# Kernel optimization log

Hardware: AMD Instinct MI355X
Metric: run time of the kernel (lower is better)

The kernel has to match this reference:

```python
import jax, jax.numpy as jnp
import numpy as np

N_NODES = 100000
N_EDGES = 1600000
N_GRAPHS = 256
D = 128
L = 3
N_OUT = 10


def setup_inputs() -> dict:
    key = jax.random.key(0)
    ks = jax.random.split(key, 6)
    x = jax.random.normal(ks[0], (N_NODES, D), dtype=jnp.float32)
    edge_index = jax.random.randint(ks[1], (2, N_EDGES), 0, N_NODES, dtype=jnp.int64)
    batch = jnp.sort(jax.random.randint(ks[2], (N_NODES,), 0, N_GRAPHS, dtype=jnp.int64))
    conv_w = jax.random.normal(ks[3], (L, D, D), dtype=jnp.float32) * (1.0 / np.sqrt(D))
    conv_b = jnp.zeros((L, D), dtype=jnp.float32)
    out_w = jax.random.normal(ks[4], (3 * D, N_OUT), dtype=jnp.float32) * (1.0 / np.sqrt(3 * D))
    out_b = jnp.zeros((N_OUT,), dtype=jnp.float32)
    return {"x": x, "edge_index": edge_index, "batch": batch,
            "conv_w": conv_w, "conv_b": conv_b, "out_w": out_w, "out_b": out_b}


def reference(x, edge_index, batch, conv_w, conv_b, out_w, out_b):
    N = x.shape[0]
    # --- add self-loops (PyG GCNConv default) ---
    loop = jnp.arange(N, dtype=edge_index.dtype)
    src = jnp.concatenate([edge_index[0], loop])  # [E+N]
    dst = jnp.concatenate([edge_index[1], loop])
    # --- symmetric normalization: deg computed on dst (col) ---
    deg = jax.ops.segment_sum(jnp.ones_like(dst, dtype=x.dtype), dst, num_segments=N)
    dinv = jnp.where(deg > 0, jax.lax.rsqrt(jnp.maximum(deg, 1.0)), 0.0)
    norm = dinv[src] * dinv[dst]  # [E+N]

    h = x
    for l in range(conv_w.shape[0]):
        h = h @ conv_w[l]                                   # [N, D] transform first
        msg = h[src] * norm[:, None]                        # gather + scale
        h = jax.ops.segment_sum(msg, dst, num_segments=N)   # scatter-add
        h = jax.nn.relu(h + conv_b[l])

    # --- global max / mean / add pooling over graphs ---
    B = N_GRAPHS
    gmax = jax.ops.segment_max(h, batch, num_segments=B)
    gsum = jax.ops.segment_sum(h, batch, num_segments=B)
    cnt = jax.ops.segment_sum(jnp.ones((N, 1), h.dtype), batch, num_segments=B)
    gmean = gsum / jnp.maximum(cnt, 1.0)
    pooled = jnp.concatenate([gmax, gmean, gsum], axis=1)   # [B, 3D]
    # dropout p=0.5 is identity in eval mode
    return pooled @ out_w + out_b
```

## Files before the change

### kernel.cpp

```cpp
#include <hip/hip_runtime.h>
#include <hip/hip_bf16.h>

#define D 128
#define NP 8
#define DPB 64
#define KPB (DPB * NP)
#define SUB 64
#define CAP_SUB 64
#define DSUB 64

typedef __attribute__((ext_vector_type(8))) __bf16 bf16x8;
typedef __attribute__((ext_vector_type(4))) float f32x4;
typedef __attribute__((ext_vector_type(4))) short s16x4;
typedef __attribute__((ext_vector_type(8))) short s16x8;

static __device__ __forceinline__ short f2bf(float f) {
    union { float f; unsigned u; } in; in.f = f;
    unsigned u = in.u;
    u += 0x7fffu + ((u >> 16) & 1u);
    return (short)(u >> 16);
}

__global__ void k_bucket(const int* __restrict__ src, const int* __restrict__ dst,
                         int* __restrict__ bcnt, int* __restrict__ staging,
                         int E, int KBE) {
    int i = blockIdx.x * 256 + threadIdx.x;
    if (i >= E) return;
    int d = dst[i], s = src[i];
    int b = d >> 6;
    int key = ((d & 63) << 3) | (s >> 14);
    int j = blockIdx.x & (SUB - 1);
    int slot = atomicAdd(&bcnt[j * KBE + b], 1);
    if (slot < CAP_SUB) staging[((size_t)j * KBE + b) * CAP_SUB + slot] = (key << 17) | s;
}

__global__ void k_btot(const int* __restrict__ bcnt, int* __restrict__ btot, int KBE) {
    int b = blockIdx.x * 256 + threadIdx.x;
    if (b >= KBE) return;
    int v = 0;
    #pragma unroll
    for (int j = 0; j < SUB; j++) {
        int c = bcnt[j * KBE + b];
        v += (c > CAP_SUB) ? CAP_SUB : c;
    }
    btot[b] = v;
}

__global__ void k_bscan(const int* __restrict__ btot, int* __restrict__ bbase,
                        int* __restrict__ row_ptr, int nkeys, int KBE) {
    __shared__ int sm[512];
    __shared__ int carry;
    int t = threadIdx.x;
    if (t == 0) carry = 0;
    __syncthreads();
    for (int c0 = 0; c0 < KBE; c0 += 512) {
        int b = c0 + t;
        int v = (b < KBE) ? btot[b] : 0;
        sm[t] = v;
        __syncthreads();
        for (int off = 1; off < 512; off <<= 1) {
            int x = (t >= off) ? sm[t - off] : 0;
            __syncthreads();
            sm[t] += x;
            __syncthreads();
        }
        if (b < KBE) bbase[b] = sm[t] - v + carry;
        __syncthreads();
        if (t == 0) carry += sm[511];
        __syncthreads();
    }
    if (t == 0) { bbase[KBE] = carry; row_ptr[nkeys] = carry; }
}

__global__ __launch_bounds__(256) void k_build(
    const int* __restrict__ staging, const int* __restrict__ bcnt,
    const int* __restrict__ bbase, int* __restrict__ row_ptr,
    int* __restrict__ csr_src, float* __restrict__ dinv,
    int* __restrict__ deg_arr, int* __restrict__ dsub, int N, int KBE)
{
    const int b = blockIdx.x;
    const int tid = threadIdx.x;
    __shared__ int cnt[KPB];
    __shared__ int subn[SUB];
    __shared__ int chunkbuf[256];
    __shared__ int carry;

    if (tid < SUB) {
        int c = bcnt[tid * KBE + b];
        subn[tid] = (c > CAP_SUB) ? CAP_SUB : c;
    }
    for (int k = tid; k < KPB; k += 256) cnt[k] = 0;
    if (tid == 0) carry = 0;
    __syncthreads();

    const int base = bbase[b];
    const int nb = bbase[b + 1] - base;
    const int j = tid >> 2, l4 = tid & 3;
    const int* __restrict__ sreg = staging + ((size_t)j * KBE + b) * CAP_SUB;
    const int sn = subn[j];

    for (int e = l4; e < sn; e += 4)
        atomicAdd(&cnt[sreg[e] >> 17], 1);
    __syncthreads();

    #pragma unroll 1
    for (int c = 0; c < KPB / 256; c++) {
        int idx = c * 256 + tid;
        int v = cnt[idx];
        chunkbuf[tid] = v;
        __syncthreads();
        for (int off = 1; off < 256; off <<= 1) {
            int x = (tid >= off) ? chunkbuf[tid - off] : 0;
            __syncthreads();
            chunkbuf[tid] += x;
            __syncthreads();
        }
        cnt[idx] = chunkbuf[tid] - v + carry;
        __syncthreads();
        if (tid == 255) carry += chunkbuf[255];
        __syncthreads();
    }

    for (int k = tid; k < KPB; k += 256)
        row_ptr[(size_t)b * KPB + k] = base + cnt[k];
    for (int dl = tid; dl < DPB; dl += 256) {
        int d = b * DPB + dl;
        if (d < N) {
            int hi2 = (dl == DPB - 1) ? nb : cnt[(dl + 1) * NP];
            int deg = hi2 - cnt[dl * NP];
            dinv[d] = rsqrtf((float)deg + 1.0f);
            int dc = (deg > 255) ? 255 : deg;
            deg_arr[d] = dc;
            atomicAdd(&dsub[((b & (DSUB - 1)) << 8) + dc], 1);
        }
    }
    __syncthreads();

    for (int e = l4; e < sn; e += 4) {
        int w = sreg[e];
        int slot = base + atomicAdd(&cnt[w >> 17], 1);
        csr_src[slot] = w & 0x1FFFF;
    }
}

__global__ void k_dscan(const int* __restrict__ dsub, int* __restrict__ dcur) {
    __shared__ int sm[256];
    const int d = threadIdx.x;
    int tot = 0;
    for (int jj = 0; jj < DSUB; jj++) tot += dsub[(jj << 8) + d];
    sm[d] = tot;
    __syncthreads();
    for (int off = 1; off < 256; off <<= 1) {
        int x = (d >= off) ? sm[d - off] : 0;
        __syncthreads();
        sm[d] += x;
        __syncthreads();
    }
    int run = sm[d] - tot;
    for (int jj = 0; jj < DSUB; jj++) {
        dcur[(jj << 8) + d] = run;
        run += dsub[(jj << 8) + d];
    }
}

__global__ void k_dscat(const int* __restrict__ deg_arr, int* __restrict__ dcur,
                        int* __restrict__ perm, int N) {
    int i = blockIdx.x * 256 + threadIdx.x;
    if (i >= N) return;
    int dc = deg_arr[i];
    int jj = (i >> 6) & (DSUB - 1);
    int pos = atomicAdd(&dcur[(jj << 8) + dc], 1);
    perm[pos] = i;
}

__global__ void k_gseg(const int* __restrict__ batch, int* __restrict__ gstart,
                       int* __restrict__ gcnt, int N, int B) {
    int g = blockIdx.x * blockDim.x + threadIdx.x;
    if (g > B) return;
    int lo = 0, hi = N;
    while (lo < hi) {
        int mid = (lo + hi) >> 1;
        if (batch[mid] < g) lo = mid + 1; else hi = mid;
    }
    gstart[g] = lo;
    if (g < B) {
        int lo2 = lo, hi2 = N;
        while (lo2 < hi2) {
            int mid = (lo2 + hi2) >> 1;
            if (batch[mid] < g + 1) lo2 = mid + 1; else hi2 = mid;
        }
        gcnt[g] = lo2 - lo;
    }
}

__global__ void k_cvt_x(const float* __restrict__ x, const float* __restrict__ dinv,
                        short* __restrict__ xb, int total4) {
    int i = blockIdx.x * blockDim.x + threadIdx.x;
    if (i < total4) {
        float d = dinv[i >> 5];
        float4 v = ((const float4*)x)[i];
        s16x4 o;
        o.x = f2bf(v.x * d); o.y = f2bf(v.y * d);
        o.z = f2bf(v.z * d); o.w = f2bf(v.w * d);
        ((s16x4*)xb)[i] = o;
    }
}

__global__ void k_cvt_w(const float* __restrict__ W, short* __restrict__ Wt, int total) {
    int i = blockIdx.x * blockDim.x + threadIdx.x;
    if (i < total) {
        int l = i >> 14;
        int rem = i & 16383;
        int n = rem >> 7;
        int k = rem & 127;
        Wt[i] = f2bf(W[(l << 14) + (k << 7) + n]);
    }
}

__global__ __launch_bounds__(256) void k_layer(
    const short* __restrict__ hin, const int* __restrict__ row_ptr,
    const int* __restrict__ csr_src, const float* __restrict__ dinv,
    const int* __restrict__ perm,
    const short* __restrict__ Wt, const float* __restrict__ bias,
    short* __restrict__ hout, float* __restrict__ hrelu, int N, int mode)
{
    __shared__ __align__(16) short tile[16 * 128];
    const int tid = threadIdx.x;
    const int wave = tid >> 6;
    const int lane = tid & 63;
    const int group = lane >> 4;
    const int lg = lane & 15;
    const int off = lg * 8;
    const int node_base = blockIdx.x * 16;
    const int r = wave * 4 + group;
    const int ti = node_base + r;

    short* dstp = &tile[r * 128 + ((lg ^ (r & 7)) << 3)];
    if (ti < N) {
        const int i = perm[ti];
        float acc[8];
        bf16x8 v = *(const bf16x8*)(hin + (size_t)i * D + off);
        #pragma unroll
        for (int k = 0; k < 8; k++) acc[k] = (float)v[k];

        int t = row_ptr[i * NP];
        const int end = row_ptr[i * NP + NP];
        for (; t + 4 <= end; t += 4) {
            int i0 = csr_src[t + 0], i1 = csr_src[t + 1];
            int i2 = csr_src[t + 2], i3 = csr_src[t + 3];
            bf16x8 v0 = *(const bf16x8*)(hin + (size_t)i0 * D + off);
            bf16x8 v1 = *(const bf16x8*)(hin + (size_t)i1 * D + off);
            bf16x8 v2 = *(const bf16x8*)(hin + (size_t)i2 * D + off);
            bf16x8 v3 = *(const bf16x8*)(hin + (size_t)i3 * D + off);
            #pragma unroll
            for (int k = 0; k < 8; k++)
                acc[k] += (((float)v0[k] + (float)v1[k]) + ((float)v2[k] + (float)v3[k]));
        }
        for (; t < end; t++) {
            int i0 = csr_src[t];
            bf16x8 v0 = *(const bf16x8*)(hin + (size_t)i0 * D + off);
            #pragma unroll
            for (int k = 0; k < 8; k++) acc[k] += (float)v0[k];
        }

        const float di = dinv[i];
        s16x8 o;
        #pragma unroll
        for (int k = 0; k < 8; k++) o[k] = f2bf(acc[k] * di);
        *(s16x8*)dstp = o;
    } else {
        s16x8 z = {0, 0, 0, 0, 0, 0, 0, 0};
        *(s16x8*)dstp = z;
    }
    __syncthreads();

    bf16x8 afrag[4];
    #pragma unroll
    for (int kt = 0; kt < 4; kt++)
        afrag[kt] = *(const bf16x8*)(&tile[lg * 128 + (((group + 4 * kt) ^ (lg & 7)) << 3)]);

    f32x4 acc2[2];
    #pragma unroll
    for (int nt = 0; nt < 2; nt++) { f32x4 z = {0.f, 0.f, 0.f, 0.f}; acc2[nt] = z; }
    #pragma unroll
    for (int nt = 0; nt < 2; nt++) {
        const short* bp = Wt + (size_t)(wave * 32 + nt * 16 + lg) * D + group * 8;
        #pragma unroll
        for (int kt = 0; kt < 4; kt++) {
            bf16x8 b = *(const bf16x8*)(bp + kt * 32);
            acc2[nt] = __builtin_amdgcn_mfma_f32_16x16x32_bf16(afrag[kt], b, acc2[nt], 0, 0, 0);
        }
    }

    float bcol[2];
    #pragma unroll
    for (int nt = 0; nt < 2; nt++) bcol[nt] = bias[wave * 32 + nt * 16 + lg];
    const int row0 = node_base + group * 4;
    #pragma unroll
    for (int i2 = 0; i2 < 4; i2++) {
        int r2 = row0 + i2;
        if (r2 < N) {
            const int n2 = perm[r2];
            if (mode == 0) {
                float dr = dinv[n2];
                #pragma unroll
                for (int nt = 0; nt < 2; nt++) {
                    int col = wave * 32 + nt * 16 + lg;
                    float val = fmaxf(acc2[nt][i2] + bcol[nt], 0.0f);
                    hout[(size_t)n2 * D + col] = f2bf(val * dr);
                }
            } else {
                #pragma unroll
                for (int nt = 0; nt < 2; nt++) {
                    int col = wave * 32 + nt * 16 + lg;
                    hrelu[(size_t)n2 * D + col] = fmaxf(acc2[nt][i2] + bcol[nt], 0.0f);
                }
            }
        }
    }
}

__global__ __launch_bounds__(256) void k_pool(const float* __restrict__ hrelu,
                                              const int* __restrict__ gstart,
                                              const int* __restrict__ gcnt,
                                              float* __restrict__ pmax,
                                              float* __restrict__ psum, int B) {
    int g = blockIdx.x >> 2;
    int q = blockIdx.x & 3;
    int c = threadIdx.x & 127;
    int p = threadIdx.x >> 7;
    int start = gstart[g];
    int endr = start + gcnt[g];

    float mx0 = 0.f, mx1 = 0.f, sm0 = 0.f, sm1 = 0.f;
    int r = start + q * 2 + p;
    for (; r + 8 < endr; r += 16) {
        float v0 = hrelu[(size_t)r * D + c];
        float v1 = hrelu[(size_t)(r + 8) * D + c];
        mx0 = fmaxf(mx0, v0); sm0 += v0;
        mx1 = fmaxf(mx1, v1); sm1 += v1;
    }
    if (r < endr) {
        float v0 = hrelu[(size_t)r * D + c];
        mx0 = fmaxf(mx0, v0); sm0 += v0;
    }
    float mx = fmaxf(mx0, mx1), sm = sm0 + sm1;

    __shared__ float smx[128], ssm[128];
    if (p == 1) { smx[c] = mx; ssm[c] = sm; }
    __syncthreads();
    if (p == 0) {
        pmax[((size_t)q * B + g) * D + c] = fmaxf(mx, smx[c]);
        psum[((size_t)q * B + g) * D + c] = sm + ssm[c];
    }
}

__global__ void k_final(const float* __restrict__ pmax, const float* __restrict__ psum,
                        const int* __restrict__ gcnt, const float* __restrict__ ow,
                        const float* __restrict__ ob, float* __restrict__ out, int B) {
    int g = blockIdx.x;
    int t = threadIdx.x;
    float part[10];
    #pragma unroll
    for (int o = 0; o < 10; o++) part[o] = 0.f;
    float invc = 1.0f / fmaxf((float)gcnt[g], 1.0f);
    for (int k = t; k < 3 * D; k += 64) {
        int c = (k < D) ? k : ((k < 2 * D) ? k - D : k - 2 * D);
        float pk;
        if (k < D) {
            float m = pmax[(size_t)g * D + c];
            #pragma unroll
            for (int q = 1; q < 4; q++) m = fmaxf(m, pmax[((size_t)q * B + g) * D + c]);
            pk = m;
        } else {
            float s = psum[(size_t)g * D + c];
            #pragma unroll
            for (int q = 1; q < 4; q++) s += psum[((size_t)q * B + g) * D + c];
            pk = (k < 2 * D) ? s * invc : s;
        }
        const float* w = ow + k * 10;
        #pragma unroll
        for (int o = 0; o < 10; o++) part[o] += pk * w[o];
    }
    #pragma unroll
    for (int off = 32; off > 0; off >>= 1)
        #pragma unroll
        for (int o = 0; o < 10; o++) part[o] += __shfl_down(part[o], off, 64);
    if (t == 0)
        #pragma unroll
        for (int o = 0; o < 10; o++) out[g * 10 + o] = part[o] + ob[o];
}

extern "C" void kernel_launch(void* const* d_in, const int* in_sizes, int n_in,
                              void* d_out, int out_size, void* d_ws, size_t ws_size,
                              hipStream_t stream) {
    const float* x     = (const float*)d_in[0];
    const int*   ei    = (const int*)d_in[1];
    const int*   batch = (const int*)d_in[2];
    const float* convw = (const float*)d_in[3];
    const float* convb = (const float*)d_in[4];
    const float* outw  = (const float*)d_in[5];
    const float* outb  = (const float*)d_in[6];
    float* out = (float*)d_out;

    const int N = in_sizes[0] / D;
    const int E = in_sizes[1] / 2;
    const int L = in_sizes[3] / (D * D);
    const int B = out_size / 10;

    const int* src = ei;
    const int* dst = ei + E;

    const int KBE   = (N + DPB - 1) / DPB;
    const int nkeys = KBE * KPB;

    char* p = (char*)d_ws;
    auto alloc = [&](size_t bytes) { char* r = p; p += (bytes + 255) & ~255ull; return r; };
    short* hb0     = (short*)alloc((size_t)N * D * 2);
    short* hb1     = (short*)alloc((size_t)N * D * 2);
    float* hrelu   = (float*)alloc((size_t)N * D * 4);
    short* Wt      = (short*)alloc((size_t)L * D * D * 2);
    int*   row_ptr = (int*)alloc(((size_t)nkeys + 1) * 4);
    int*   csr_src = (int*)alloc((size_t)E * 4);
    int*   bcnt    = (int*)alloc((size_t)SUB * KBE * 4);
    int*   btot    = (int*)alloc((size_t)KBE * 4);
    int*   bbase   = (int*)alloc(((size_t)KBE + 1) * 4);
    float* dinv    = (float*)alloc((size_t)N * 4);
    float* pmax    = (float*)alloc((size_t)4 * B * D * 4);
    float* psum    = (float*)alloc((size_t)4 * B * D * 4);
    int*   gcnt    = (int*)alloc((size_t)B * 4);
    int*   gstart  = (int*)alloc(((size_t)B + 1) * 4);
    int*   deg_arr = (int*)alloc((size_t)N * 4);
    int*   dsub    = (int*)alloc((size_t)DSUB * 256 * 4);
    int*   dcur    = (int*)alloc((size_t)DSUB * 256 * 4);
    int*   perm    = (int*)alloc((size_t)N * 4);

    int* staging = (int*)hrelu;

    hipMemsetAsync(bcnt, 0, (size_t)SUB * KBE * 4, stream);
    hipMemsetAsync(dsub, 0, (size_t)DSUB * 256 * 4, stream);

    k_bucket<<<(E + 255) / 256, 256, 0, stream>>>(src, dst, bcnt, staging, E, KBE);
    k_gseg<<<1, 512, 0, stream>>>(batch, gstart, gcnt, N, B);
    k_btot<<<(KBE + 255) / 256, 256, 0, stream>>>(bcnt, btot, KBE);
    k_bscan<<<1, 512, 0, stream>>>(btot, bbase, row_ptr, nkeys, KBE);
    k_build<<<KBE, 256, 0, stream>>>(staging, bcnt, bbase, row_ptr, csr_src, dinv,
                                     deg_arr, dsub, N, KBE);
    k_dscan<<<1, 256, 0, stream>>>(dsub, dcur);
    k_dscat<<<(N + 255) / 256, 256, 0, stream>>>(deg_arr, dcur, perm, N);
    k_cvt_x<<<((N * D / 4) + 255) / 256, 256, 0, stream>>>(x, dinv, hb0, N * D / 4);
    k_cvt_w<<<((L * D * D) + 255) / 256, 256, 0, stream>>>(convw, Wt, L * D * D);

    const int lblocks = (N + 15) / 16;
    k_layer<<<lblocks, 256, 0, stream>>>(hb0, row_ptr, csr_src, dinv, perm, Wt,
                                         convb, hb1, hrelu, N, 0);
    k_layer<<<lblocks, 256, 0, stream>>>(hb1, row_ptr, csr_src, dinv, perm, Wt + D * D,
                                         convb + D, hb0, hrelu, N, 0);
    k_layer<<<lblocks, 256, 0, stream>>>(hb0, row_ptr, csr_src, dinv, perm, Wt + 2 * D * D,
                                         convb + 2 * D, hb1, hrelu, N, 1);

    k_pool<<<B * 4, 256, 0, stream>>>(hrelu, gstart, gcnt, pmax, psum, B);
    k_final<<<B, 64, 0, stream>>>(pmax, psum, gcnt, outw, outb, out, B);
}
```

Measured before the change: 476.9 us.

## Process 64 nodes per layer block with round-robin degree-balanced permutation

The fused aggregate+GEMM layer kernel now handles 64 nodes per block instead of 16. Each wave gathers four node rows in sequence, then runs the MFMA transform on a 16-row slice against all 128 output columns in two halves. The degree-sorted permutation is dealt round-robin across blocks so each block gets a similar mix of degrees, and padding slots are marked -1 by a memset. This cuts block count and per-block weight-load overhead and is meant to balance gather work across blocks. In exchange, each block uses more LDS and more accumulator registers, and occupancy is requested via launch bounds.

```diff
diff --git a/kernel.cpp b/kernel.cpp
--- a/kernel.cpp
+++ b/kernel.cpp
@@ -8,6 +8,7 @@
 #define SUB 64
 #define CAP_SUB 64
 #define DSUB 64
+#define NBLK 64
 
 typedef __attribute__((ext_vector_type(8))) __bf16 bf16x8;
 typedef __attribute__((ext_vector_type(4))) float f32x4;
@@ -164,13 +165,15 @@
 }
 
 __global__ void k_dscat(const int* __restrict__ deg_arr, int* __restrict__ dcur,
-                        int* __restrict__ perm, int N) {
+                        int* __restrict__ perm, int N, int LB) {
     int i = blockIdx.x * 256 + threadIdx.x;
     if (i >= N) return;
     int dc = deg_arr[i];
     int jj = (i >> 6) & (DSUB - 1);
     int pos = atomicAdd(&dcur[(jj << 8) + dc], 1);
-    perm[pos] = i;
+    int blk = pos % LB;
+    int q = pos / LB;
+    perm[blk * NBLK + q] = i;
 }
 
 __global__ void k_gseg(const int* __restrict__ batch, int* __restrict__ gstart,
@@ -217,103 +220,108 @@
     }
 }
 
-__global__ __launch_bounds__(256) void k_layer(
+__global__ __launch_bounds__(256, 8) void k_layer(
     const short* __restrict__ hin, const int* __restrict__ row_ptr,
     const int* __restrict__ csr_src, const float* __restrict__ dinv,
     const int* __restrict__ perm,
     const short* __restrict__ Wt, const float* __restrict__ bias,
     short* __restrict__ hout, float* __restrict__ hrelu, int N, int mode)
 {
-    __shared__ __align__(16) short tile[16 * 128];
+    __shared__ __align__(16) short tile[NBLK * 128];
     const int tid = threadIdx.x;
     const int wave = tid >> 6;
     const int lane = tid & 63;
     const int group = lane >> 4;
     const int lg = lane & 15;
     const int off = lg * 8;
-    const int node_base = blockIdx.x * 16;
-    const int r = wave * 4 + group;
-    const int ti = node_base + r;
-
-    short* dstp = &tile[r * 128 + ((lg ^ (r & 7)) << 3)];
-    if (ti < N) {
-        const int i = perm[ti];
-        float acc[8];
-        bf16x8 v = *(const bf16x8*)(hin + (size_t)i * D + off);
-        #pragma unroll
-        for (int k = 0; k < 8; k++) acc[k] = (float)v[k];
-
-        int t = row_ptr[i * NP];
-        const int end = row_ptr[i * NP + NP];
-        for (; t + 4 <= end; t += 4) {
-            int i0 = csr_src[t + 0], i1 = csr_src[t + 1];
-            int i2 = csr_src[t + 2], i3 = csr_src[t + 3];
-            bf16x8 v0 = *(const bf16x8*)(hin + (size_t)i0 * D + off);
-            bf16x8 v1 = *(const bf16x8*)(hin + (size_t)i1 * D + off);
-            bf16x8 v2 = *(const bf16x8*)(hin + (size_t)i2 * D + off);
-            bf16x8 v3 = *(const bf16x8*)(hin + (size_t)i3 * D + off);
+    const int gidx = wave * 4 + group;
+    const int base_ti = blockIdx.x * NBLK;
+
+    #pragma unroll 1
+    for (int rd = 0; rd < 4; rd++) {
+        const int ln = rd * 16 + gidx;
+        const int i = perm[base_ti + ln];
+        short* dstp = &tile[ln * 128 + ((lg ^ (ln & 7)) << 3)];
+        if (i >= 0) {
+            float acc[8];
+            bf16x8 v = *(const bf16x8*)(hin + (size_t)i * D + off);
             #pragma unroll
-            for (int k = 0; k < 8; k++)
-                acc[k] += (((float)v0[k] + (float)v1[k]) + ((float)v2[k] + (float)v3[k]));
-        }
-        for (; t < end; t++) {
-            int i0 = csr_src[t];
-            bf16x8 v0 = *(const bf16x8*)(hin + (size_t)i0 * D + off);
+            for (int k = 0; k < 8; k++) acc[k] = (float)v[k];
+
+            int t = row_ptr[i * NP];
+            const int end = row_ptr[i * NP + NP];
+            for (; t + 4 <= end; t += 4) {
+                int i0 = csr_src[t + 0], i1 = csr_src[t + 1];
+                int i2 = csr_src[t + 2], i3 = csr_src[t + 3];
+                bf16x8 v0 = *(const bf16x8*)(hin + (size_t)i0 * D + off);
+                bf16x8 v1 = *(const bf16x8*)(hin + (size_t)i1 * D + off);
+                bf16x8 v2 = *(const bf16x8*)(hin + (size_t)i2 * D + off);
+                bf16x8 v3 = *(const bf16x8*)(hin + (size_t)i3 * D + off);
+                #pragma unroll
+                for (int k = 0; k < 8; k++)
+                    acc[k] += (((float)v0[k] + (float)v1[k]) + ((float)v2[k] + (float)v3[k]));
+            }
+            for (; t < end; t++) {
+                int i0 = csr_src[t];
+                bf16x8 v0 = *(const bf16x8*)(hin + (size_t)i0 * D + off);
+                #pragma unroll
+                for (int k = 0; k < 8; k++) acc[k] += (float)v0[k];
+            }
+
+            const float di = dinv[i];
+            s16x8 o;
             #pragma unroll
-            for (int k = 0; k < 8; k++) acc[k] += (float)v0[k];
-        }
-
-        const float di = dinv[i];
-        s16x8 o;
-        #pragma unroll
-        for (int k = 0; k < 8; k++) o[k] = f2bf(acc[k] * di);
-        *(s16x8*)dstp = o;
-    } else {
-        s16x8 z = {0, 0, 0, 0, 0, 0, 0, 0};
-        *(s16x8*)dstp = z;
-    }
-    __syncthreads();
-
-    bf16x8 afrag[4];
+            for (int k = 0; k < 8; k++) o[k] = f2bf(acc[k] * di);
+            *(s16x8*)dstp = o;
+        } else {
+            s16x8 z = {0, 0, 0, 0, 0, 0, 0, 0};
+            *(s16x8*)dstp = z;
+        }
+    }
+    __syncthreads();
+
+    bf16x8 aa[4];
+    const int R = wave * 16 + lg;
     #pragma unroll
     for (int kt = 0; kt < 4; kt++)
-        afrag[kt] = *(const bf16x8*)(&tile[lg * 128 + (((group + 4 * kt) ^ (lg & 7)) << 3)]);
-
-    f32x4 acc2[2];
-    #pragma unroll
-    for (int nt = 0; nt < 2; nt++) { f32x4 z = {0.f, 0.f, 0.f, 0.f}; acc2[nt] = z; }
-    #pragma unroll
-    for (int nt = 0; nt < 2; nt++) {
-        const short* bp = Wt + (size_t)(wave * 32 + nt * 16 + lg) * D + group * 8;
-        #pragma unroll
-        for (int kt = 0; kt < 4; kt++) {
-            bf16x8 b = *(const bf16x8*)(bp + kt * 32);
-            acc2[nt] = __builtin_amdgcn_mfma_f32_16x16x32_bf16(afrag[kt], b, acc2[nt], 0, 0, 0);
-        }
-    }
-
-    float bcol[2];
-    #pragma unroll
-    for (int nt = 0; nt < 2; nt++) bcol[nt] = bias[wave * 32 + nt * 16 + lg];
-    const int row0 = node_base + group * 4;
-    #pragma unroll
-    for (int i2 = 0; i2 < 4; i2++) {
-        int r2 = row0 + i2;
-        if (r2 < N) {
-            const int n2 = perm[r2];
-            if (mode == 0) {
-                float dr = dinv[n2];
-                #pragma unroll
-                for (int nt = 0; nt < 2; nt++) {
-                    int col = wave * 32 + nt * 16 + lg;
-                    float val = fmaxf(acc2[nt][i2] + bcol[nt], 0.0f);
-                    hout[(size_t)n2 * D + col] = f2bf(val * dr);
-                }
-            } else {
-                #pragma unroll
-                for (int nt = 0; nt < 2; nt++) {
-                    int col = wave * 32 + nt * 16 + lg;
-                    hrelu[(size_t)n2 * D + col] = fmaxf(acc2[nt][i2] + bcol[nt], 0.0f);
+        aa[kt] = *(const bf16x8*)(&tile[R * 128 + (((group + 4 * kt) ^ (R & 7)) << 3)]);
+
+    #pragma unroll 1
+    for (int half = 0; half < 2; half++) {
+        f32x4 acc2[4];
+        #pragma unroll
+        for (int ct = 0; ct < 4; ct++) { f32x4 z = {0.f, 0.f, 0.f, 0.f}; acc2[ct] = z; }
+        #pragma unroll
+        for (int ct = 0; ct < 4; ct++) {
+            const short* bp = Wt + (size_t)((half * 4 + ct) * 16 + lg) * D + group * 8;
+            #pragma unroll
+            for (int kt = 0; kt < 4; kt++) {
+                bf16x8 b = *(const bf16x8*)(bp + kt * 32);
+                acc2[ct] = __builtin_amdgcn_mfma_f32_16x16x32_bf16(aa[kt], b, acc2[ct], 0, 0, 0);
+            }
+        }
+        float bcol[4];
+        #pragma unroll
+        for (int ct = 0; ct < 4; ct++) bcol[ct] = bias[(half * 4 + ct) * 16 + lg];
+
+        #pragma unroll
+        for (int i2 = 0; i2 < 4; i2++) {
+            const int lrow = wave * 16 + group * 4 + i2;
+            const int n2 = perm[base_ti + lrow];
+            if (n2 >= 0) {
+                if (mode == 0) {
+                    const float dr = dinv[n2];
+                    #pragma unroll
+                    for (int ct = 0; ct < 4; ct++) {
+                        float val = fmaxf(acc2[ct][i2] + bcol[ct], 0.0f);
+                        hout[(size_t)n2 * D + (half * 4 + ct) * 16 + lg] = f2bf(val * dr);
+                    }
+                } else {
+                    #pragma unroll
+                    for (int ct = 0; ct < 4; ct++) {
+                        hrelu[(size_t)n2 * D + (half * 4 + ct) * 16 + lg] =
+                            fmaxf(acc2[ct][i2] + bcol[ct], 0.0f);
+                    }
                 }
             }
         }
@@ -413,6 +421,7 @@
 
     const int KBE   = (N + DPB - 1) / DPB;
     const int nkeys = KBE * KPB;
+    const int LB    = (N + NBLK - 1) / NBLK;
 
     char* p = (char*)d_ws;
     auto alloc = [&](size_t bytes) { char* r = p; p += (bytes + 255) & ~255ull; return r; };
@@ -433,12 +442,13 @@
     int*   deg_arr = (int*)alloc((size_t)N * 4);
     int*   dsub    = (int*)alloc((size_t)DSUB * 256 * 4);
     int*   dcur    = (int*)alloc((size_t)DSUB * 256 * 4);
-    int*   perm    = (int*)alloc((size_t)N * 4);
+    int*   perm    = (int*)alloc((size_t)LB * NBLK * 4);
 
     int* staging = (int*)hrelu;
 
     hipMemsetAsync(bcnt, 0, (size_t)SUB * KBE * 4, stream);
     hipMemsetAsync(dsub, 0, (size_t)DSUB * 256 * 4, stream);
+    hipMemsetAsync(perm, 0xFF, (size_t)LB * NBLK * 4, stream);
 
     k_bucket<<<(E + 255) / 256, 256, 0, stream>>>(src, dst, bcnt, staging, E, KBE);
     k_gseg<<<1, 512, 0, stream>>>(batch, gstart, gcnt, N, B);
@@ -447,17 +457,16 @@
     k_build<<<KBE, 256, 0, stream>>>(staging, bcnt, bbase, row_ptr, csr_src, dinv,
                                      deg_arr, dsub, N, KBE);
     k_dscan<<<1, 256, 0, stream>>>(dsub, dcur);
-    k_dscat<<<(N + 255) / 256, 256, 0, stream>>>(deg_arr, dcur, perm, N);
+    k_dscat<<<(N + 255) / 256, 256, 0, stream>>>(deg_arr, dcur, perm, N, LB);
     k_cvt_x<<<((N * D / 4) + 255) / 256, 256, 0, stream>>>(x, dinv, hb0, N * D / 4);
     k_cvt_w<<<((L * D * D) + 255) / 256, 256, 0, stream>>>(convw, Wt, L * D * D);
 
-    const int lblocks = (N + 15) / 16;
-    k_layer<<<lblocks, 256, 0, stream>>>(hb0, row_ptr, csr_src, dinv, perm, Wt,
-                                         convb, hb1, hrelu, N, 0);
-    k_layer<<<lblocks, 256, 0, stream>>>(hb1, row_ptr, csr_src, dinv, perm, Wt + D * D,
-                                         convb + D, hb0, hrelu, N, 0);
-    k_layer<<<lblocks, 256, 0, stream>>>(hb0, row_ptr, csr_src, dinv, perm, Wt + 2 * D * D,
-                                         convb + 2 * D, hb1, hrelu, N, 1);
+    k_layer<<<LB, 256, 0, stream>>>(hb0, row_ptr, csr_src, dinv, perm, Wt,
+                                    convb, hb1, hrelu, N, 0);
+    k_layer<<<LB, 256, 0, stream>>>(hb1, row_ptr, csr_src, dinv, perm, Wt + D * D,
+                                    convb + D, hb0, hrelu, N, 0);
+    k_layer<<<LB, 256, 0, stream>>>(hb0, row_ptr, csr_src, dinv, perm, Wt + 2 * D * D,
+                                    convb + 2 * D, hb1, hrelu, N, 1);
 
     k_pool<<<B * 4, 256, 0, stream>>>(hrelu, gstart, gcnt, pmax, psum, B);
     k_final<<<B, 64, 0, stream>>>(pmax, psum, gcnt, outw, outb, out, B);
```

Result: slower. 520.3 us (+9.1%).
